# Performance work log

Measured on AMD Instinct MI355X. Metric: run time of the kernel, lower is better.

## Reference

```python
import jax, jax.numpy as jnp
import numpy as np

WIN = 11      # pytorch_msssim default win_size
SIGMA = 1.5   # pytorch_msssim default win_sigma
K1, K2 = 0.01, 0.03
DATA_RANGE = 1.0


def _gauss_win():
    coords = np.arange(WIN, dtype=np.float64) - WIN // 2
    g = np.exp(-(coords ** 2) / (2.0 * SIGMA ** 2))
    g = g / g.sum()
    return jnp.asarray(g, dtype=jnp.float32)


def _gauss_filter(x, w):
    # x: [B, C, H, W]; separable depthwise gaussian, VALID padding (pytorch_msssim style)
    C = x.shape[1]
    dn = ('NCHW', 'OIHW', 'NCHW')
    kh = jnp.broadcast_to(w.reshape(1, 1, WIN, 1), (C, 1, WIN, 1))
    kw = jnp.broadcast_to(w.reshape(1, 1, 1, WIN), (C, 1, 1, WIN))
    x = jax.lax.conv_general_dilated(x, kh, (1, 1), 'VALID',
                                     dimension_numbers=dn, feature_group_count=C)
    x = jax.lax.conv_general_dilated(x, kw, (1, 1), 'VALID',
                                     dimension_numbers=dn, feature_group_count=C)
    return x


def _ssim_mean(X, Y):
    C1 = (K1 * DATA_RANGE) ** 2
    C2 = (K2 * DATA_RANGE) ** 2
    w = _gauss_win()
    mu1 = _gauss_filter(X, w)
    mu2 = _gauss_filter(Y, w)
    mu1_sq = mu1 * mu1
    mu2_sq = mu2 * mu2
    mu1_mu2 = mu1 * mu2
    sigma1_sq = _gauss_filter(X * X, w) - mu1_sq
    sigma2_sq = _gauss_filter(Y * Y, w) - mu2_sq
    sigma12 = _gauss_filter(X * Y, w) - mu1_mu2
    cs_map = (2.0 * sigma12 + C2) / (sigma1_sq + sigma2_sq + C2)
    ssim_map = ((2.0 * mu1_mu2 + C1) / (mu1_sq + mu2_sq + C1)) * cs_map
    return jnp.mean(ssim_map)


def setup_inputs() -> dict:
    key = jax.random.key(0)
    k1, k2 = jax.random.split(key)
    inp = jax.random.uniform(k1, (64, 1, 512, 512), dtype=jnp.float32)
    tgt = jax.random.uniform(k2, (64, 1, 512, 512), dtype=jnp.float32)
    return {"input": inp, "target": tgt}


def reference(input, target):
    # SSIMLoss.forward: 1 - SSIM(data_range=1, size_average=True, channel=1)(input, target)
    return 1.0 - _ssim_mean(input, target)
```

## Files before the change

kernel.cpp:

```cpp
#include <hip/hip_runtime.h>
#include <math.h>

#define WIN 11
#define OH 32
#define OW 64
#define VSTRH 80
#define PLANEH (OH * VSTRH)
#define IMG 512
#define OUTD 502
#define NIMG 64

typedef _Float16 h2 __attribute__((ext_vector_type(2)));
typedef _Float16 h4 __attribute__((ext_vector_type(4)));
typedef _Float16 h8 __attribute__((ext_vector_type(8)));
typedef __fp16   fp16x2 __attribute__((ext_vector_type(2)));

struct GW { unsigned whp[WIN]; };

union U32H2 { unsigned u; h2 h; fp16x2 f; };
__device__ inline h2 wsplat(unsigned u) { U32H2 x; x.u = u; return x.h; }
__device__ inline h2 alignh(h2 hi, h2 lo) {
    U32H2 a, b, r; a.h = lo; b.h = hi;
    r.u = (a.u >> 16) | (b.u << 16);
    return r.h;
}
__device__ inline h2 pkrtz(float a, float b) {
    U32H2 x; x.f = __builtin_amdgcn_cvt_pkrtz(a, b); return x.h;
}

__global__ __launch_bounds__(64) void ssim_zero(double* acc) {
    if (threadIdx.x == 0) acc[0] = 0.0;
}

__global__ __launch_bounds__(256, 3) void ssim_kernel(
    const float* __restrict__ X, const float* __restrict__ Y,
    double* __restrict__ acc, GW gw)
{
    __shared__ _Float16 vb[5 * PLANEH];
    __shared__ float red[4];

    const int tid = threadIdx.x;
    const int tC = blockIdx.x, tR = blockIdx.y, b = blockIdx.z;
    const int gr0 = tR * OH, gc0 = tC * OW;
    const float* __restrict__ Xb = X + (size_t)b * (IMG * IMG);
    const float* __restrict__ Yb = Y + (size_t)b * (IMG * IMG);

    if (tid < 152) {
        const int rg = tid / 19, cg = tid - rg * 19;
        const int r0 = rg * 4;
        int gc = gc0 + cg * 4;
        if (gc > IMG - 4) gc = IMG - 4;

        h2 a[5][4][2] = {};
        #pragma unroll
        for (int k = 0; k < 4 + WIN - 1; ++k) {
            int gr = gr0 + r0 + k; if (gr > IMG - 1) gr = IMG - 1;
            const float4 xv = *reinterpret_cast<const float4*>(Xb + (size_t)gr * IMG + gc);
            const float4 yv = *reinterpret_cast<const float4*>(Yb + (size_t)gr * IMG + gc);
            h2 x0 = pkrtz(xv.x, xv.y);
            h2 x1 = pkrtz(xv.z, xv.w);
            h2 y0 = pkrtz(yv.x, yv.y);
            h2 y1 = pkrtz(yv.z, yv.w);
            h2 xx0 = x0 * x0, xx1 = x1 * x1;
            h2 yy0 = y0 * y0, yy1 = y1 * y1;
            h2 xy0 = x0 * y0, xy1 = x1 * y1;
            #pragma unroll
            for (int i2 = 0; i2 < 4; ++i2) {
                const int t = k - i2;
                if (t >= 0 && t < WIN) {
                    const h2 wt = wsplat(gw.whp[t]);
                    a[0][i2][0] += wt * x0;  a[0][i2][1] += wt * x1;
                    a[1][i2][0] += wt * y0;  a[1][i2][1] += wt * y1;
                    a[2][i2][0] += wt * xx0; a[2][i2][1] += wt * xx1;
                    a[3][i2][0] += wt * yy0; a[3][i2][1] += wt * yy1;
                    a[4][i2][0] += wt * xy0; a[4][i2][1] += wt * xy1;
                }
            }
        }
        #pragma unroll
        for (int ch = 0; ch < 5; ++ch) {
            #pragma unroll
            for (int i2 = 0; i2 < 4; ++i2) {
                h4 v;
                v[0] = a[ch][i2][0][0]; v[1] = a[ch][i2][0][1];
                v[2] = a[ch][i2][1][0]; v[3] = a[ch][i2][1][1];
                *reinterpret_cast<h4*>(&vb[ch * PLANEH + (r0 + i2) * VSTRH + cg * 4]) = v;
            }
        }
    }
    __syncthreads();

    const int r   = tid >> 3;
    const int c0h = (tid & 7) * 8;
    const _Float16* rb = &vb[r * VSTRH];

    h2 m[5][4];
    #pragma unroll
    for (int ch = 0; ch < 5; ++ch) {
        const _Float16* p = rb + ch * PLANEH;
        h8 v0 = *reinterpret_cast<const h8*>(p + c0h);
        h8 v1 = *reinterpret_cast<const h8*>(p + c0h + 8);
        h2 e8 = *reinterpret_cast<const h2*>(p + c0h + 16);
        h2 e[9];
        #pragma unroll
        for (int j = 0; j < 4; ++j) e[j]     = h2{ v0[2*j], v0[2*j+1] };
        #pragma unroll
        for (int j = 0; j < 4; ++j) e[4 + j] = h2{ v1[2*j], v1[2*j+1] };
        e[8] = e8;
        h2 o[8];
        #pragma unroll
        for (int j = 0; j < 8; ++j) o[j] = alignh(e[j+1], e[j]);

        #pragma unroll
        for (int pr = 0; pr < 4; ++pr) {
            h2 s = h2{ (_Float16)0, (_Float16)0 };
            #pragma unroll
            for (int u = 0; u < 6; ++u)
                s += wsplat(gw.whp[2*u]) * e[pr + u];
            #pragma unroll
            for (int u = 0; u < 5; ++u)
                s += wsplat(gw.whp[2*u+1]) * o[pr + u];
            m[ch][pr] = s;
        }
    }

    const float C1 = 1e-4f, C2 = 9e-4f;
    float ssv[8];
    #pragma unroll
    for (int pr = 0; pr < 4; ++pr) {
        #pragma unroll
        for (int h = 0; h < 2; ++h) {
            float mu1 = (float)m[0][pr][h];
            float mu2 = (float)m[1][pr][h];
            float mu1s = mu1 * mu1, mu2s = mu2 * mu2, m12 = mu1 * mu2;
            float s1  = (float)m[2][pr][h] - mu1s;
            float s2  = (float)m[3][pr][h] - mu2s;
            float s12 = (float)m[4][pr][h] - m12;
            float num = (2.f * s12 + C2) * (2.f * m12 + C1);
            float den = (s1 + s2 + C2) * (mu1s + mu2s + C1);
            ssv[2*pr + h] = num * __builtin_amdgcn_rcpf(den);
        }
    }

    float lsum = 0.f;
    if (tR < 15 && tC < 7) {
        #pragma unroll
        for (int o = 0; o < 8; ++o) lsum += ssv[o];
    } else {
        const int ogr = gr0 + r;
        #pragma unroll
        for (int o = 0; o < 8; ++o) {
            const int ogc = gc0 + c0h + o;
            if (ogr < OUTD && ogc < OUTD) lsum += ssv[o];
        }
    }

    #pragma unroll
    for (int off = 32; off > 0; off >>= 1)
        lsum += __shfl_down(lsum, off, 64);
    if ((tid & 63) == 0) red[tid >> 6] = lsum;
    __syncthreads();
    if (tid == 0) {
        float bs = red[0] + red[1] + red[2] + red[3];
        atomicAdd(acc, (double)bs);
    }
}

__global__ void ssim_finalize(const double* __restrict__ acc,
                              float* __restrict__ out) {
    out[0] = 1.0f - (float)(acc[0] / (double)((long long)NIMG * OUTD * OUTD));
}

static unsigned short f2h_rne(float f) {
    union { float f; unsigned u; } v; v.f = f;
    unsigned u = v.u;
    unsigned s = (u >> 16) & 0x8000u;
    int e = (int)((u >> 23) & 0xff) - 112;
    unsigned mant = u & 0x7fffffu;
    unsigned h = s | ((unsigned)e << 10) | (mant >> 13);
    unsigned rem = mant & 0x1fffu;
    if (rem > 0x1000u || (rem == 0x1000u && (h & 1u))) h++;
    return (unsigned short)h;
}

extern "C" void kernel_launch(void* const* d_in, const int* in_sizes, int n_in,
                              void* d_out, int out_size, void* d_ws, size_t ws_size,
                              hipStream_t stream) {
    const float* X = (const float*)d_in[0];
    const float* Y = (const float*)d_in[1];
    double* acc = (double*)d_ws;
    float* out = (float*)d_out;

    GW gw;
    double c[WIN], s = 0.0;
    for (int i = 0; i < WIN; ++i) {
        double d = (double)i - (double)(WIN / 2);
        c[i] = exp(-(d * d) / (2.0 * 1.5 * 1.5));
        s += c[i];
    }
    for (int i = 0; i < WIN; ++i) {
        unsigned short hb = f2h_rne((float)(c[i] / s));
        gw.whp[i] = (unsigned)hb | ((unsigned)hb << 16);
    }

    ssim_zero<<<1, 64, 0, stream>>>(acc);
    dim3 grid(IMG / OW, IMG / OH, NIMG);
    ssim_kernel<<<grid, 256, 0, stream>>>(X, Y, acc, gw);
    ssim_finalize<<<1, 1, 0, stream>>>(acc, out);
}
```

Baseline: 124.6 us.

## Stage raw input tiles into LDS via global_load_lds before vertical filter

The input X/Y tile (42 rows by 76 columns per image) is first copied from global memory straight into shared memory with the async global_load_lds builtin. The vertical Gaussian pass then reads its operands from LDS. That pass is re-split into 296 work items, each covering 2 columns instead of 4, so all 256 threads take part rather than only 152. The aim is better latency hiding and more parallelism in the vertical stage. In exchange it adds about 25KB of LDS per block, which may limit occupancy, an extra barrier, and an uneven second iteration for the first 40 threads.

```diff
diff --git a/kernel.cpp b/kernel.cpp
--- a/kernel.cpp
+++ b/kernel.cpp
@@ -4,6 +4,9 @@
 #define WIN 11
 #define OH 32
 #define OW 64
+#define RROWS 42
+#define RCH 19
+#define RSTRF 76
 #define VSTRH 80
 #define PLANEH (OH * VSTRH)
 #define IMG 512
@@ -11,9 +14,11 @@
 #define NIMG 64
 
 typedef _Float16 h2 __attribute__((ext_vector_type(2)));
-typedef _Float16 h4 __attribute__((ext_vector_type(4)));
 typedef _Float16 h8 __attribute__((ext_vector_type(8)));
 typedef __fp16   fp16x2 __attribute__((ext_vector_type(2)));
+
+typedef __attribute__((address_space(3))) unsigned       lds_u32;
+typedef const __attribute__((address_space(1))) unsigned glb_u32;
 
 struct GW { unsigned whp[WIN]; };
 
@@ -27,6 +32,9 @@
 __device__ inline h2 pkrtz(float a, float b) {
     U32H2 x; x.f = __builtin_amdgcn_cvt_pkrtz(a, b); return x.h;
 }
+__device__ inline void gl_lds16(const void* g, void* l) {
+    __builtin_amdgcn_global_load_lds((glb_u32*)g, (lds_u32*)l, 16, 0, 0);
+}
 
 __global__ __launch_bounds__(64) void ssim_zero(double* acc) {
     if (threadIdx.x == 0) acc[0] = 0.0;
@@ -36,6 +44,7 @@
     const float* __restrict__ X, const float* __restrict__ Y,
     double* __restrict__ acc, GW gw)
 {
+    __shared__ float raw[2 * RROWS * RSTRF];
     __shared__ _Float16 vb[5 * PLANEH];
     __shared__ float red[4];
 
@@ -45,35 +54,42 @@
     const float* __restrict__ Xb = X + (size_t)b * (IMG * IMG);
     const float* __restrict__ Yb = Y + (size_t)b * (IMG * IMG);
 
-    if (tid < 152) {
-        const int rg = tid / 19, cg = tid - rg * 19;
+    {
+        const int totalc = 2 * RROWS * RCH;
+        for (int c = tid; c < totalc; c += 256) {
+            int img = (c >= RROWS * RCH) ? 1 : 0;
+            int rem = c - img * (RROWS * RCH);
+            int row = rem / RCH;
+            int chk = rem - row * RCH;
+            int grow = gr0 + row; if (grow > IMG - 1) grow = IMG - 1;
+            int gcol = gc0 + chk * 4; if (gcol > IMG - 4) gcol = IMG - 4;
+            const float* src = (img ? Yb : Xb) + (size_t)grow * IMG + gcol;
+            gl_lds16(src, (char*)raw + (size_t)(c & ~63) * 16);
+        }
+    }
+    __syncthreads();
+
+    for (int t = tid; t < 296; t += 256) {
+        const int rg = t / 37, cp = t - rg * 37;
         const int r0 = rg * 4;
-        int gc = gc0 + cg * 4;
-        if (gc > IMG - 4) gc = IMG - 4;
-
-        h2 a[5][4][2] = {};
+        h2 a[5][4] = {};
         #pragma unroll
         for (int k = 0; k < 4 + WIN - 1; ++k) {
-            int gr = gr0 + r0 + k; if (gr > IMG - 1) gr = IMG - 1;
-            const float4 xv = *reinterpret_cast<const float4*>(Xb + (size_t)gr * IMG + gc);
-            const float4 yv = *reinterpret_cast<const float4*>(Yb + (size_t)gr * IMG + gc);
-            h2 x0 = pkrtz(xv.x, xv.y);
-            h2 x1 = pkrtz(xv.z, xv.w);
-            h2 y0 = pkrtz(yv.x, yv.y);
-            h2 y1 = pkrtz(yv.z, yv.w);
-            h2 xx0 = x0 * x0, xx1 = x1 * x1;
-            h2 yy0 = y0 * y0, yy1 = y1 * y1;
-            h2 xy0 = x0 * y0, xy1 = x1 * y1;
+            const float2 xv = *reinterpret_cast<const float2*>(&raw[(r0 + k) * RSTRF + cp * 2]);
+            const float2 yv = *reinterpret_cast<const float2*>(&raw[RROWS * RSTRF + (r0 + k) * RSTRF + cp * 2]);
+            h2 x = pkrtz(xv.x, xv.y);
+            h2 y = pkrtz(yv.x, yv.y);
+            h2 xx = x * x, yy = y * y, xy = x * y;
             #pragma unroll
             for (int i2 = 0; i2 < 4; ++i2) {
-                const int t = k - i2;
-                if (t >= 0 && t < WIN) {
-                    const h2 wt = wsplat(gw.whp[t]);
-                    a[0][i2][0] += wt * x0;  a[0][i2][1] += wt * x1;
-                    a[1][i2][0] += wt * y0;  a[1][i2][1] += wt * y1;
-                    a[2][i2][0] += wt * xx0; a[2][i2][1] += wt * xx1;
-                    a[3][i2][0] += wt * yy0; a[3][i2][1] += wt * yy1;
-                    a[4][i2][0] += wt * xy0; a[4][i2][1] += wt * xy1;
+                const int tt = k - i2;
+                if (tt >= 0 && tt < WIN) {
+                    const h2 wt = wsplat(gw.whp[tt]);
+                    a[0][i2] += wt * x;
+                    a[1][i2] += wt * y;
+                    a[2][i2] += wt * xx;
+                    a[3][i2] += wt * yy;
+                    a[4][i2] += wt * xy;
                 }
             }
         }
@@ -81,10 +97,7 @@
         for (int ch = 0; ch < 5; ++ch) {
             #pragma unroll
             for (int i2 = 0; i2 < 4; ++i2) {
-                h4 v;
-                v[0] = a[ch][i2][0][0]; v[1] = a[ch][i2][0][1];
-                v[2] = a[ch][i2][1][0]; v[3] = a[ch][i2][1][1];
-                *reinterpret_cast<h4*>(&vb[ch * PLANEH + (r0 + i2) * VSTRH + cg * 4]) = v;
+                *reinterpret_cast<h2*>(&vb[ch * PLANEH + (r0 + i2) * VSTRH + cp * 2]) = a[ch][i2];
             }
         }
     }
```

Result: no change. 125.5 us (+0.7%).
